# Kernel tuning notes

Hardware: AMD Instinct MI355X
Metric: run time of the kernel (lower is better)

The kernel has to match this reference:

```python
import jax, jax.numpy as jnp
import numpy as np

N_BINS = 15


def setup_inputs() -> dict:
    key = jax.random.key(0)
    k1, k2 = jax.random.split(key)
    N, C = 1000000, 100
    logits = jax.random.normal(k1, (N, C), dtype=jnp.float32)
    labels = jax.random.randint(k2, (N,), 0, C, dtype=jnp.int64)
    return {"logits": logits, "labels": labels, "t_opt": 0}


def reference(logits, labels, t_opt):
    # temperature scaling branch (t_opt is a static Python int)
    scaled = logits / t_opt if t_opt != 0 else logits
    probs = jax.nn.softmax(scaled, axis=-1)            # [N, C]
    confidences = jnp.max(probs, axis=1)               # [N]
    predictions = jnp.argmax(probs, axis=1)            # [N]
    accuracies = (predictions == labels).astype(jnp.float32)

    # bin index: confidences in (bin_lower, bin_upper] -> single-pass histogram
    boundaries = jnp.linspace(0.0, 1.0, N_BINS + 1)
    bin_idx = jnp.clip(
        jnp.searchsorted(boundaries, confidences, side="left") - 1, 0, N_BINS - 1
    )

    ones = jnp.ones_like(confidences)
    counts = jax.ops.segment_sum(ones, bin_idx, num_segments=N_BINS)
    sum_conf = jax.ops.segment_sum(confidences, bin_idx, num_segments=N_BINS)
    sum_acc = jax.ops.segment_sum(accuracies, bin_idx, num_segments=N_BINS)

    n = confidences.shape[0]
    safe = jnp.maximum(counts, 1.0)
    avg_conf = sum_conf / safe
    avg_acc = sum_acc / safe
    prop = counts / n
    per_bin = jnp.where(counts > 0, jnp.abs(avg_conf - avg_acc) * prop, 0.0)
    return jnp.sum(per_bin).reshape(1)
```

## Files before the change

kernel.cpp:

```cpp
#include <hip/hip_runtime.h>
#include <math.h>

#define NBINS 15
#define TROWS 64
#define NC 100
#define F4_PER_ROW 25
#define F4_PER_TILE (TROWS * F4_PER_ROW)
#define BLOCK 256

__device__ __forceinline__ void compute_tile(
    const float4* __restrict__ buf, int r, int q, long long rbase, int labCur,
    float scale, int N, float* s_cnt, float* s_conf, float* s_acc)
{
    if (rbase + r >= N) return;
    const float4* rowp = buf + r * F4_PER_ROW;
    const int nf = (q == 0) ? 7 : 6;
    const int fb = (q == 0) ? 0 : (1 + q * 6);

    float4 v[7];
#pragma unroll
    for (int j = 0; j < 7; ++j)
        if (j < nf) v[j] = rowp[fb + j];

    float m = -INFINITY; int mi = 0;
#pragma unroll
    for (int j = 0; j < 7; ++j) if (j < nf) {
        const int cb = (fb + j) * 4;
        float4 w = v[j];
        w.x *= scale; w.y *= scale; w.z *= scale; w.w *= scale;
        v[j] = w;
        if (w.x > m) { m = w.x; mi = cb;     }
        if (w.y > m) { m = w.y; mi = cb + 1; }
        if (w.z > m) { m = w.z; mi = cb + 2; }
        if (w.w > m) { m = w.w; mi = cb + 3; }
    }
#pragma unroll
    for (int off = 1; off <= 2; off <<= 1) {
        const float om  = __shfl_xor(m, off);
        const int   omi = __shfl_xor(mi, off);
        if (om > m || (om == m && omi < mi)) { m = om; mi = omi; }
    }

    float e = 0.f;
#pragma unroll
    for (int j = 0; j < 7; ++j) if (j < nf) {
        const float4 w = v[j];
        e += __expf(w.x - m) + __expf(w.y - m)
           + __expf(w.z - m) + __expf(w.w - m);
    }
    e += __shfl_xor(e, 1);
    e += __shfl_xor(e, 2);

    if (q == 0) {
        const float conf = 1.0f / e;
        const float acc  = (mi == labCur) ? 1.0f : 0.0f;
        int jc = 0;
#pragma unroll
        for (int i = 0; i <= NBINS; ++i) {
            const float b = (float)i * (1.0f / 15.0f);
            jc += (b < conf) ? 1 : 0;
        }
        int bin = jc - 1;
        bin = bin < 0 ? 0 : (bin > NBINS - 1 ? NBINS - 1 : bin);
        atomicAdd(&s_cnt[bin],  1.0f);
        atomicAdd(&s_conf[bin], conf);
        atomicAdd(&s_acc[bin],  acc);
    }
}

__global__ __launch_bounds__(BLOCK, 3) void ece_main(const float* __restrict__ logits,
                                                     const int* __restrict__ labels,
                                                     const int* __restrict__ t_opt,
                                                     float* __restrict__ gbins,
                                                     int N) {
    __shared__ float4 s_tile[2][F4_PER_TILE];
    __shared__ float s_cnt[NBINS], s_conf[NBINS], s_acc[NBINS];

    const int tid = threadIdx.x;
    if (tid < NBINS) { s_cnt[tid] = 0.f; s_conf[tid] = 0.f; s_acc[tid] = 0.f; }

    const int lane   = tid & 63;
    const int wv     = tid >> 6;
    const int wvBase = wv * 400;
    const int r      = tid >> 2;
    const int q      = tid & 3;

    const int tt = t_opt[0];
    float scale = (tt != 0) ? (1.0f / (float)tt) : 1.0f;
    asm volatile("" :: "v"(scale));

    const float4* __restrict__ lg4 = (const float4*)logits;
    const long long lim = (long long)N * F4_PER_ROW - 1;
    const int nTiles = (N + TROWS - 1) / TROWS;
    const int stride = gridDim.x;

    float4 sA0, sA1, sA2, sA3, sA4, sA5, sA6;  int labsA = 0;
    float4 sB0, sB1, sB2, sB3, sB4, sB5, sB6;  int labsB = 0;

#define CLK(kk) ((kk) < lim ? (kk) : lim)
#define ISSUE(P, tile) do {                                                   \
    const long long tb_ = (long long)(tile) * F4_PER_TILE + wvBase + lane;    \
    P##0 = lg4[CLK(tb_)];                                                     \
    P##1 = lg4[CLK(tb_ + 64)];                                                \
    P##2 = lg4[CLK(tb_ + 128)];                                               \
    P##3 = lg4[CLK(tb_ + 192)];                                               \
    P##4 = lg4[CLK(tb_ + 256)];                                               \
    P##5 = lg4[CLK(tb_ + 320)];                                               \
    if (lane < 16) P##6 = lg4[CLK(tb_ + 384)];                                \
    if (q == 0) {                                                             \
        long long rr_ = (long long)(tile) * TROWS + (tid >> 2);               \
        lab##P = labels[rr_ < N ? rr_ : (N - 1)];                             \
    }                                                                          \
} while (0)

#define DSW(P, b) do {                                                        \
    float4* d_ = &s_tile[b][wvBase + lane];                                   \
    d_[0]   = P##0; d_[64]  = P##1; d_[128] = P##2;                           \
    d_[192] = P##3; d_[256] = P##4; d_[320] = P##5;                           \
    if (lane < 16) d_[384] = P##6;                                            \
} while (0)

#define VMW8  asm volatile("s_waitcnt vmcnt(8)" ::: "memory")
#define VMW0  asm volatile("s_waitcnt vmcnt(0)" ::: "memory")
#define LGKM0 asm volatile("s_waitcnt lgkmcnt(0)" ::: "memory")
#define SB    __builtin_amdgcn_sched_barrier(0)
#define BAR   __builtin_amdgcn_s_barrier()

    int  t     = blockIdx.x;
    bool vCur  = (t < nTiles);
    bool vNext = (t + stride < nTiles);
    int  cur   = 0;

    if (vCur)  ISSUE(sA, t);
    if (vNext) ISSUE(sB, t + stride);
    if (vCur) {
        if (vNext) VMW8; else VMW0;
        SB;
        DSW(sA, 0);
    }
    LGKM0; SB; BAR; SB;

    if (vCur) for (;;) {
        {
            const int  tn2 = t + 2 * stride;
            const bool v2  = tn2 < nTiles;
            const int  labCur = labsA;
            if (v2) ISSUE(sA, tn2);
            compute_tile(s_tile[cur], r, q, (long long)t * TROWS, labCur,
                         scale, N, s_cnt, s_conf, s_acc);
            if (vNext) {
                if (v2) VMW8; else VMW0;
                SB;
                DSW(sB, cur ^ 1);
            }
            LGKM0; SB; BAR; SB;
            vCur = vNext; vNext = v2; t += stride; cur ^= 1;
            if (!vCur) break;
        }
        {
            const int  tn2 = t + 2 * stride;
            const bool v2  = tn2 < nTiles;
            const int  labCur = labsB;
            if (v2) ISSUE(sB, tn2);
            compute_tile(s_tile[cur], r, q, (long long)t * TROWS, labCur,
                         scale, N, s_cnt, s_conf, s_acc);
            if (vNext) {
                if (v2) VMW8; else VMW0;
                SB;
                DSW(sA, cur ^ 1);
            }
            LGKM0; SB; BAR; SB;
            vCur = vNext; vNext = v2; t += stride; cur ^= 1;
            if (!vCur) break;
        }
    }

    VMW0;
    __syncthreads();
    if (tid < NBINS) {
        atomicAdd(&gbins[tid],             s_cnt[tid]);
        atomicAdd(&gbins[NBINS + tid],     s_conf[tid]);
        atomicAdd(&gbins[2 * NBINS + tid], s_acc[tid]);
    }
#undef CLK
#undef ISSUE
#undef DSW
#undef VMW8
#undef VMW0
#undef LGKM0
#undef SB
#undef BAR
}

__global__ void ece_final(const float* __restrict__ gbins,
                          float* __restrict__ out, int N) {
    if (threadIdx.x == 0 && blockIdx.x == 0) {
        float ece = 0.f;
        for (int b = 0; b < NBINS; ++b) {
            const float c = gbins[b];
            if (c > 0.f) {
                const float avg_conf = gbins[NBINS + b] / c;
                const float avg_acc  = gbins[2 * NBINS + b] / c;
                ece += fabsf(avg_conf - avg_acc) * (c / (float)N);
            }
        }
        out[0] = ece;
    }
}

extern "C" void kernel_launch(void* const* d_in, const int* in_sizes, int n_in,
                              void* d_out, int out_size, void* d_ws, size_t ws_size,
                              hipStream_t stream) {
    const float* logits = (const float*)d_in[0];
    const int*   labels = (const int*)d_in[1];
    const int*   t_opt  = (const int*)d_in[2];
    float* out   = (float*)d_out;
    float* gbins = (float*)d_ws;

    const int N = in_sizes[1];

    hipMemsetAsync(gbins, 0, 3 * NBINS * sizeof(float), stream);

    const int nTiles = (N + TROWS - 1) / TROWS;
    const int blocks = nTiles < 768 ? nTiles : 768;
    ece_main<<<blocks, BLOCK, 0, stream>>>(logits, labels, t_opt, gbins, N);
    ece_final<<<1, 64, 0, stream>>>(gbins, out, N);
}
```

Baseline: 95.28 us.

## Make each wavefront own private 16-row chunks and drop block barriers

After: 96.76 us. No clear change (+1.6%).

```diff
diff --git a/kernel.cpp b/kernel.cpp
--- a/kernel.cpp
+++ b/kernel.cpp
@@ -2,18 +2,17 @@
 #include <math.h>
 
 #define NBINS 15
-#define TROWS 64
-#define NC 100
-#define F4_PER_ROW 25
-#define F4_PER_TILE (TROWS * F4_PER_ROW)
+#define CROWS 16
+#define F4C   (CROWS * 25)
 #define BLOCK 256
-
-__device__ __forceinline__ void compute_tile(
+#define WPB   (BLOCK / 64)
+
+__device__ __forceinline__ void compute_chunk(
     const float4* __restrict__ buf, int r, int q, long long rbase, int labCur,
     float scale, int N, float* s_cnt, float* s_conf, float* s_acc)
 {
     if (rbase + r >= N) return;
-    const float4* rowp = buf + r * F4_PER_ROW;
+    const float4* rowp = buf + r * 25;
     const int nf = (q == 0) ? 7 : 6;
     const int fb = (q == 0) ? 0 : (1 + q * 6);
 
@@ -73,48 +72,43 @@
                                                      const int* __restrict__ t_opt,
                                                      float* __restrict__ gbins,
                                                      int N) {
-    __shared__ float4 s_tile[2][F4_PER_TILE];
+    __shared__ float4 s_tile[WPB][2][F4C];
     __shared__ float s_cnt[NBINS], s_conf[NBINS], s_acc[NBINS];
 
-    const int tid = threadIdx.x;
+    const int tid  = threadIdx.x;
+    const int lane = tid & 63;
+    const int wv   = tid >> 6;
+    const int r    = lane >> 2;
+    const int q    = lane & 3;
+
     if (tid < NBINS) { s_cnt[tid] = 0.f; s_conf[tid] = 0.f; s_acc[tid] = 0.f; }
-
-    const int lane   = tid & 63;
-    const int wv     = tid >> 6;
-    const int wvBase = wv * 400;
-    const int r      = tid >> 2;
-    const int q      = tid & 3;
+    __syncthreads();
 
     const int tt = t_opt[0];
     float scale = (tt != 0) ? (1.0f / (float)tt) : 1.0f;
     asm volatile("" :: "v"(scale));
 
     const float4* __restrict__ lg4 = (const float4*)logits;
-    const long long lim = (long long)N * F4_PER_ROW - 1;
-    const int nTiles = (N + TROWS - 1) / TROWS;
-    const int stride = gridDim.x;
+    const int limF4   = N * 25 - 1;
+    const int nChunks = (N + CROWS - 1) / CROWS;
+    const int stride  = gridDim.x * WPB;
 
     float4 sA0, sA1, sA2, sA3, sA4, sA5, sA6;  int labsA = 0;
     float4 sB0, sB1, sB2, sB3, sB4, sB5, sB6;  int labsB = 0;
 
-#define CLK(kk) ((kk) < lim ? (kk) : lim)
-#define ISSUE(P, tile) do {                                                   \
-    const long long tb_ = (long long)(tile) * F4_PER_TILE + wvBase + lane;    \
-    P##0 = lg4[CLK(tb_)];                                                     \
-    P##1 = lg4[CLK(tb_ + 64)];                                                \
-    P##2 = lg4[CLK(tb_ + 128)];                                               \
-    P##3 = lg4[CLK(tb_ + 192)];                                               \
-    P##4 = lg4[CLK(tb_ + 256)];                                               \
-    P##5 = lg4[CLK(tb_ + 320)];                                               \
-    if (lane < 16) P##6 = lg4[CLK(tb_ + 384)];                                \
-    if (q == 0) {                                                             \
-        long long rr_ = (long long)(tile) * TROWS + (tid >> 2);               \
-        lab##P = labels[rr_ < N ? rr_ : (N - 1)];                             \
-    }                                                                          \
+#define CLK(k) ((k) < limF4 ? (k) : limF4)
+#define ISSUE(P, cc) do {                                                     \
+    const int b_ = (cc) * F4C + lane;                                         \
+    P##0 = lg4[CLK(b_)];       P##1 = lg4[CLK(b_ + 64)];                      \
+    P##2 = lg4[CLK(b_ + 128)]; P##3 = lg4[CLK(b_ + 192)];                     \
+    P##4 = lg4[CLK(b_ + 256)]; P##5 = lg4[CLK(b_ + 320)];                     \
+    if (lane < 16) P##6 = lg4[CLK(b_ + 384)];                                 \
+    if (q == 0) { const int rr_ = (cc) * CROWS + r;                           \
+                  lab##P = labels[rr_ < N ? rr_ : N - 1]; }                   \
 } while (0)
 
 #define DSW(P, b) do {                                                        \
-    float4* d_ = &s_tile[b][wvBase + lane];                                   \
+    float4* d_ = &s_tile[wv][b][lane];                                        \
     d_[0]   = P##0; d_[64]  = P##1; d_[128] = P##2;                           \
     d_[192] = P##3; d_[256] = P##4; d_[320] = P##5;                           \
     if (lane < 16) d_[384] = P##6;                                            \
@@ -123,54 +117,53 @@
 #define VMW8  asm volatile("s_waitcnt vmcnt(8)" ::: "memory")
 #define VMW0  asm volatile("s_waitcnt vmcnt(0)" ::: "memory")
 #define LGKM0 asm volatile("s_waitcnt lgkmcnt(0)" ::: "memory")
-#define SB    __builtin_amdgcn_sched_barrier(0)
-#define BAR   __builtin_amdgcn_s_barrier()
-
-    int  t     = blockIdx.x;
-    bool vCur  = (t < nTiles);
-    bool vNext = (t + stride < nTiles);
+#define SBR   __builtin_amdgcn_sched_barrier(0)
+
+    int  c     = blockIdx.x * WPB + wv;
+    bool vCur  = (c < nChunks);
+    bool vNext = (c + stride < nChunks);
     int  cur   = 0;
 
-    if (vCur)  ISSUE(sA, t);
-    if (vNext) ISSUE(sB, t + stride);
+    if (vCur)  ISSUE(sA, c);
+    if (vNext) ISSUE(sB, c + stride);
     if (vCur) {
         if (vNext) VMW8; else VMW0;
-        SB;
+        SBR;
         DSW(sA, 0);
-    }
-    LGKM0; SB; BAR; SB;
+        LGKM0; SBR;
+    }
 
     if (vCur) for (;;) {
         {
-            const int  tn2 = t + 2 * stride;
-            const bool v2  = tn2 < nTiles;
+            const int  cn2 = c + 2 * stride;
+            const bool v2  = cn2 < nChunks;
             const int  labCur = labsA;
-            if (v2) ISSUE(sA, tn2);
-            compute_tile(s_tile[cur], r, q, (long long)t * TROWS, labCur,
-                         scale, N, s_cnt, s_conf, s_acc);
+            if (v2) ISSUE(sA, cn2);
+            compute_chunk(&s_tile[wv][cur][0], r, q, (long long)c * CROWS,
+                          labCur, scale, N, s_cnt, s_conf, s_acc);
             if (vNext) {
                 if (v2) VMW8; else VMW0;
-                SB;
+                SBR;
                 DSW(sB, cur ^ 1);
+                LGKM0; SBR;
             }
-            LGKM0; SB; BAR; SB;
-            vCur = vNext; vNext = v2; t += stride; cur ^= 1;
+            vCur = vNext; vNext = v2; c += stride; cur ^= 1;
             if (!vCur) break;
         }
         {
-            const int  tn2 = t + 2 * stride;
-            const bool v2  = tn2 < nTiles;
+            const int  cn2 = c + 2 * stride;
+            const bool v2  = cn2 < nChunks;
             const int  labCur = labsB;
-            if (v2) ISSUE(sB, tn2);
-            compute_tile(s_tile[cur], r, q, (long long)t * TROWS, labCur,
-                         scale, N, s_cnt, s_conf, s_acc);
+            if (v2) ISSUE(sB, cn2);
+            compute_chunk(&s_tile[wv][cur][0], r, q, (long long)c * CROWS,
+                          labCur, scale, N, s_cnt, s_conf, s_acc);
             if (vNext) {
                 if (v2) VMW8; else VMW0;
-                SB;
+                SBR;
                 DSW(sA, cur ^ 1);
+                LGKM0; SBR;
             }
-            LGKM0; SB; BAR; SB;
-            vCur = vNext; vNext = v2; t += stride; cur ^= 1;
+            vCur = vNext; vNext = v2; c += stride; cur ^= 1;
             if (!vCur) break;
         }
     }
@@ -188,8 +181,7 @@
 #undef VMW8
 #undef VMW0
 #undef LGKM0
-#undef SB
-#undef BAR
+#undef SBR
 }
 
 __global__ void ece_final(const float* __restrict__ gbins,
@@ -221,8 +213,9 @@
 
     hipMemsetAsync(gbins, 0, 3 * NBINS * sizeof(float), stream);
 
-    const int nTiles = (N + TROWS - 1) / TROWS;
-    const int blocks = nTiles < 768 ? nTiles : 768;
+    const int nChunks = (N + CROWS - 1) / CROWS;
+    int blocks = (nChunks + WPB - 1) / WPB;
+    if (blocks > 768) blocks = 768;
     ece_main<<<blocks, BLOCK, 0, stream>>>(logits, labels, t_opt, gbins, N);
     ece_final<<<1, 64, 0, stream>>>(gbins, out, N);
 }
```
